# Optimization experiments

Hardware: AMD Instinct MI355X
Metric: run time of the kernel (lower is better)

Reference implementation:

```python
import jax, jax.numpy as jnp
import numpy as np

N_USER = 100000
N_ITEM = 100000
SUPP = 10000
B = 1024
L = 50
S = 256
H = 4
E = 64
HID = 64


def setup_inputs() -> dict:
    key = jax.random.key(0)
    ks = jax.random.split(key, 32)
    f32 = jnp.float32
    inp = {}
    # forward int args
    inp["x"] = jax.random.randint(ks[0], (B, 2), 0, N_USER)
    inp["src_his"] = jax.random.randint(ks[1], (B, L), 0, N_ITEM)
    inp["src_hl"] = jax.random.randint(ks[2], (B,), 0, L)
    inp["tgt_his"] = jax.random.randint(ks[3], (B, L), 0, N_ITEM)
    inp["tgt_hl"] = jax.random.randint(ks[4], (B,), 0, L)
    # precomputed neighbor sampling: [2 get_user_emb calls, H heads, B, S]
    inp["sample_idx"] = jax.random.randint(ks[5], (2, H, B, S), 0, SUPP)
    inp["supp_users"] = jax.random.randint(ks[6], (SUPP,), 0, N_USER)
    # embedding tables (xavier-ish small scale)
    inp["src_user_emb"] = jax.random.normal(ks[7], (N_USER, E), f32) * 0.1
    inp["src_item_emb"] = jax.random.normal(ks[8], (N_ITEM, E), f32) * 0.1
    inp["tgt_user_emb"] = jax.random.normal(ks[9], (N_USER, E), f32) * 0.1
    inp["tgt_item_emb"] = jax.random.normal(ks[10], (N_ITEM, E), f32) * 0.1
    # attention / aggregation weights, stored [in, out]
    s = 1.0 / np.sqrt(E)
    inp["W_att_w"] = jax.random.normal(ks[11], (E, E), f32) * s
    inp["W_att_b"] = jnp.full((E,), 0.1, f32)
    inp["W_agg_w"] = jax.random.normal(ks[12], (E, E), f32) * s
    # per-head GAT projections, batched over heads
    inp["Wq"] = jax.random.normal(ks[13], (H, E, E), f32) * s
    inp["Wk"] = jax.random.normal(ks[14], (H, E, E), f32) * s
    inp["Wv"] = jax.random.normal(ks[15], (H, E, E), f32) * s
    inp["W_out"] = jax.random.normal(ks[16], (H * E, E), f32) * (1.0 / np.sqrt(H * E))
    # scoring MLP
    inp["l1_w"] = jax.random.normal(ks[17], (2 * E, HID), f32) * (1.0 / np.sqrt(2 * E))
    inp["l1_b"] = jnp.full((HID,), 0.1, f32)
    inp["l2_w"] = jax.random.normal(ks[18], (HID, E), f32) * (1.0 / np.sqrt(HID))
    inp["l2_b"] = jnp.full((E,), 0.1, f32)
    inp["l3_w"] = jax.random.normal(ks[19], (E, 1), f32) * s
    inp["l3_b"] = jnp.full((1,), 0.1, f32)
    return inp


def reference(x, src_his, src_hl, tgt_his, tgt_hl, sample_idx, supp_users,
              src_user_emb, src_item_emb, tgt_user_emb, tgt_item_emb,
              W_att_w, W_att_b, W_agg_w, Wq, Wk, Wv, W_out,
              l1_w, l1_b, l2_w, l2_b, l3_w, l3_b):
    user_id = x[:, 0]
    item_id = x[:, 1]

    def user_fea_encode(his, hl, user_table):
        # NOTE: original always gathers from src_model.item_embedding (even for tgt)
        Lh = his.shape[1]
        valid = jnp.arange(Lh)[None, :] < hl[:, None]          # [B,L]
        hist = src_item_emb[his] * valid[..., None]             # [B,L,E], padded rows zeroed
        u = user_table[user_id]                                 # [B,E]
        keyt = jnp.tanh(hist @ W_att_w + W_att_b)               # [B,L,E]
        pad = hist.sum(-1) == 0                                 # [B,L]
        att = jnp.einsum('ble,be->bl', keyt, u)
        # faithful masked_softmax: masked scores set to 0 BEFORE exp (exp(0)=1 still contributes)
        att = jnp.where(pad, 0.0, att)
        e = jnp.exp(att)
        att = e / (jnp.sum(e, axis=1, keepdims=True) + 1e-12)
        out = jnp.einsum('bl,ble->be', att, hist)
        return out @ W_agg_w                                    # W_agg has no bias

    def get_user_emb(fea, idx):
        # idx: [H,B,S] indices into supp_users; all heads batched in one einsum chain
        neigh = tgt_user_emb[supp_users[idx]]                   # [H,B,S,E]
        q = jnp.einsum('be,heo->hbo', fea, Wq)                  # [H,B,O]
        k = jnp.einsum('hbse,heo->hbso', neigh, Wk)             # [H,B,S,O]
        attn = jax.nn.softmax(jnp.einsum('hbo,hbso->hbs', q, k), axis=-1)
        ctx = jnp.einsum('hbs,hbso->hbo', attn, k)              # weighted sum over neighbors
        g = jnp.einsum('hbo,hop->hbp', ctx, Wv)                 # [H,B,O]
        g = jnp.transpose(g, (1, 0, 2)).reshape(fea.shape[0], -1)  # concat heads -> [B,H*O]
        return g @ W_out

    user_src_fea = user_fea_encode(src_his, src_hl, src_user_emb)
    user_emb = get_user_emb(user_src_fea, sample_idx[0])
    item_emb = tgt_item_emb[item_id]
    user_tgt_fea = user_fea_encode(tgt_his, tgt_hl, tgt_user_emb)
    hybrid_tgt_emb = get_user_emb(user_tgt_fea, sample_idx[1])

    x_t = jnp.concatenate([hybrid_tgt_emb, item_emb], axis=1)
    x1_t = jnp.tanh(x_t @ l1_w + l1_b)
    x2_t = jnp.tanh(x1_t @ l2_w + l2_b)
    x3_t = (x2_t @ l3_w + l3_b).reshape(-1)

    output = jnp.sum(user_emb * item_emb, axis=1)
    out_emb_s = user_emb * item_emb
    # (output, output_t, out_emb_s, out_emb_t); train=False branch (sim/domain heads are None)
    return (output, x3_t, out_emb_s, x2_t)
```

## Files before the change

### kernel.cpp

```cpp
#include <hip/hip_runtime.h>

constexpr int B    = 1024;
constexpr int L    = 50;
constexpr int S    = 256;
constexpr int H    = 4;
constexpr int E    = 64;
constexpr int HID  = 64;
constexpr int SUPP = 10000;

__device__ __forceinline__ float lanebc(float v, int l) {
    return __int_as_float(__builtin_amdgcn_readlane(__float_as_int(v), l));
}

__global__ __launch_bounds__(256) void encode_kernel(
    const int* __restrict__ x,
    const int* __restrict__ src_his,
    const int* __restrict__ src_hl,
    const int* __restrict__ tgt_his,
    const int* __restrict__ tgt_hl,
    const float* __restrict__ item_emb,
    const float* __restrict__ src_user_emb,
    const float* __restrict__ tgt_user_emb,
    const float* __restrict__ W_att_w,
    const float* __restrict__ W_att_b,
    const float* __restrict__ W_agg_w,
    float* __restrict__ fea_out)
{
    __shared__ float sHist[L * E];
    __shared__ float sAtt[L];
    __shared__ float sPart[4][E];
    __shared__ float sOut[E];

    const int b    = blockIdx.x;
    const int call = blockIdx.y;
    const int tid  = threadIdx.x;
    const int lane = tid & 63;
    const int wave = tid >> 6;

    const int* his = call ? tgt_his : src_his;
    const int* hl  = call ? tgt_hl  : src_hl;
    const float* user_table = call ? tgt_user_emb : src_user_emb;

    float wcol[E];
#pragma unroll
    for (int i = 0; i < E; i++) wcol[i] = W_att_w[i * E + lane];

    const int uid   = x[2 * b];
    const float uv  = user_table[(size_t)uid * E + lane];
    const float bias = W_att_b[lane];
    const int hlen  = hl[b];

    for (int l = wave; l < L; l += 4) {
        const int it = his[b * L + l];
        const float hv = (l < hlen) ? item_emb[(size_t)it * E + lane] : 0.0f;
        sHist[l * E + lane] = hv;
        float a = bias;
#pragma unroll
        for (int i = 0; i < E; i++) a += lanebc(hv, i) * wcol[i];
        float part = tanhf(a) * uv;
        float hsum = hv;
#pragma unroll
        for (int off = 32; off; off >>= 1) {
            part += __shfl_xor(part, off);
            hsum += __shfl_xor(hsum, off);
        }
        if (lane == 0) sAtt[l] = (hsum == 0.0f) ? 0.0f : part;
    }
    __syncthreads();

    if (wave == 0) {
        float v = (lane < L) ? expf(sAtt[lane]) : 0.0f;
        float s = v;
#pragma unroll
        for (int off = 32; off; off >>= 1) s += __shfl_xor(s, off);
        const float denom = s + 1e-12f;
        if (lane < L) sAtt[lane] = v / denom;
    }
    __syncthreads();

    float c = 0.0f;
    for (int l = wave; l < L; l += 4) c += sAtt[l] * sHist[l * E + lane];
    sPart[wave][lane] = c;
    __syncthreads();
    if (tid < E) sOut[tid] = sPart[0][tid] + sPart[1][tid] + sPart[2][tid] + sPart[3][tid];
    __syncthreads();

    float g = 0.0f;
#pragma unroll
    for (int k = 0; k < 16; k++) {
        const int i = wave * 16 + k;
        g += sOut[i] * W_agg_w[i * E + lane];
    }
    sPart[wave][lane] = g;
    __syncthreads();
    if (wave == 0) {
        fea_out[((size_t)call * B + b) * E + lane] =
            sPart[0][lane] + sPart[1][lane] + sPart[2][lane] + sPart[3][lane];
    }
}

__global__ __launch_bounds__(256) void ksupp_kernel(
    const int* __restrict__ supp_users,
    const float* __restrict__ tgt_user_emb,
    const float* __restrict__ Wk,
    float* __restrict__ K_supp)
{
    const int tid  = threadIdx.x;
    const int lane = tid & 63;
    const int h    = tid >> 6;

    float wcol[E];
#pragma unroll
    for (int i = 0; i < E; i++) wcol[i] = Wk[h * E * E + i * E + lane];

#pragma unroll 2
    for (int j = blockIdx.x; j < SUPP; j += gridDim.x) {
        const int u = supp_users[j];
        const float ev = tgt_user_emb[(size_t)u * E + lane];
        float acc = 0.0f;
#pragma unroll
        for (int i = 0; i < E; i++) acc += lanebc(ev, i) * wcol[i];
        K_supp[((size_t)h * SUPP + j) * E + lane] = acc;
    }
}

__global__ __launch_bounds__(256) void q_kernel(
    const float* __restrict__ fea,
    const float* __restrict__ Wq,
    float* __restrict__ qout)
{
    const int tid  = threadIdx.x;
    const int lane = tid & 63;
    const int h    = tid >> 6;
    const int call = blockIdx.y;

    float wcol[E];
#pragma unroll
    for (int i = 0; i < E; i++) wcol[i] = Wq[h * E * E + i * E + lane];

    for (int b = blockIdx.x; b < B; b += gridDim.x) {
        const float fv = fea[((size_t)call * B + b) * E + lane];
        float acc = 0.0f;
#pragma unroll
        for (int i = 0; i < E; i++) acc += lanebc(fv, i) * wcol[i];
        qout[(((call * H) + h) * B + b) * E + lane] = acc;
    }
}

__global__ __launch_bounds__(256) void attn_kernel(
    const int* __restrict__ sample_idx,
    const float* __restrict__ K_supp,
    const float* __restrict__ qarr,
    const float* __restrict__ Wv,
    float* __restrict__ gout)
{
    __shared__ float sK[S * E];
    __shared__ float sP[S];
    __shared__ float sRed[8];
    __shared__ float sCtx[4][E];
    __shared__ float sC[E];
    __shared__ float sG[4][E];

    const int b    = blockIdx.x;
    const int h    = blockIdx.y;
    const int call = blockIdx.z;
    const int tid  = threadIdx.x;
    const int lane = tid & 63;
    const int wave = tid >> 6;

    const int* idx = sample_idx + (((call * H) + h) * B + b) * S;
    const float* Kh = K_supp + (size_t)h * SUPP * E;
    const float qv = qarr[(((call * H) + h) * B + b) * E + lane];

    const int s0   = wave * 64;
    const int u    = lane & 15;
    const int rsub = lane >> 4;
#pragma unroll
    for (int i = 0; i < 16; i++) {
        const int r = s0 + i * 4 + rsub;
        const int j = idx[r];
        const float4 kv = *(const float4*)(Kh + (size_t)j * E + u * 4);
        *(float4*)(sK + r * 64 + ((u ^ (r & 15)) << 2)) = kv;
    }
    __syncthreads();

    const int tmask = tid & 15;
    float acc = 0.0f;
#pragma unroll
    for (int uu = 0; uu < 16; uu++) {
        const float4 kv = *(const float4*)(sK + tid * 64 + (((uu ^ tmask)) << 2));
        acc += kv.x * lanebc(qv, 4 * uu)
             + kv.y * lanebc(qv, 4 * uu + 1)
             + kv.z * lanebc(qv, 4 * uu + 2)
             + kv.w * lanebc(qv, 4 * uu + 3);
    }

    float m = acc;
#pragma unroll
    for (int off = 32; off; off >>= 1) m = fmaxf(m, __shfl_xor(m, off));
    if (lane == 0) sRed[wave] = m;
    __syncthreads();
    const float mx = fmaxf(fmaxf(sRed[0], sRed[1]), fmaxf(sRed[2], sRed[3]));
    const float ex = expf(acc - mx);
    float sm = ex;
#pragma unroll
    for (int off = 32; off; off >>= 1) sm += __shfl_xor(sm, off);
    if (lane == 0) sRed[4 + wave] = sm;
    __syncthreads();
    const float denom = sRed[4] + sRed[5] + sRed[6] + sRed[7];
    sP[tid] = ex / denom;
    __syncthreads();

    float4 cacc = make_float4(0.0f, 0.0f, 0.0f, 0.0f);
    const int sbase = s0 + (lane >> 4) * 16;
#pragma unroll
    for (int i = 0; i < 16; i++) {
        const int s = sbase + i;
        const float ps = sP[s];
        const float4 kv = *(const float4*)(sK + s * 64 + ((u ^ (s & 15)) << 2));
        cacc.x += ps * kv.x;
        cacc.y += ps * kv.y;
        cacc.z += ps * kv.z;
        cacc.w += ps * kv.w;
    }
#pragma unroll
    for (int off = 16; off <= 32; off <<= 1) {
        cacc.x += __shfl_xor(cacc.x, off);
        cacc.y += __shfl_xor(cacc.y, off);
        cacc.z += __shfl_xor(cacc.z, off);
        cacc.w += __shfl_xor(cacc.w, off);
    }
    if (lane < 16) *(float4*)(&sCtx[wave][u * 4]) = cacc;
    __syncthreads();
    if (wave == 0) {
        sC[lane] = sCtx[0][lane] + sCtx[1][lane] + sCtx[2][lane] + sCtx[3][lane];
    }
    __syncthreads();

    const float* Wvh = Wv + h * E * E;
    float g = 0.0f;
#pragma unroll
    for (int k = 0; k < 16; k++) {
        const int c = wave * 16 + k;
        g += sC[c] * Wvh[c * E + lane];
    }
    sG[wave][lane] = g;
    __syncthreads();
    if (wave == 0) {
        gout[((size_t)(call * B) + b) * (H * E) + h * E + lane] =
            sG[0][lane] + sG[1][lane] + sG[2][lane] + sG[3][lane];
    }
}

__global__ __launch_bounds__(256) void final_kernel(
    const int* __restrict__ x,
    const float* __restrict__ tgt_item_emb,
    const float* __restrict__ gsrc,
    const float* __restrict__ gtgt,
    const float* __restrict__ W_out,
    const float* __restrict__ l1_w,
    const float* __restrict__ l1_b,
    const float* __restrict__ l2_w,
    const float* __restrict__ l2_b,
    const float* __restrict__ l3_w,
    const float* __restrict__ l3_b,
    float* __restrict__ out)
{
    __shared__ float sPart[4][E];
    __shared__ float sHyb[E];
    __shared__ float sItem[E];
    __shared__ float sX1[HID];

    const int b    = blockIdx.x;
    const int tid  = threadIdx.x;
    const int lane = tid & 63;
    const int wave = tid >> 6;

    if (tid < E) {
        const int item = x[2 * b + 1];
        sItem[tid] = tgt_item_emb[(size_t)item * E + tid];
    }

    const float* grow = (wave < 2) ? (gsrc + (size_t)b * (H * E))
                                   : (gtgt + (size_t)b * (H * E));
    const int i0 = (wave & 1) * 128;
    float acc = 0.0f;
    for (int i = i0; i < i0 + 128; i++) {
        acc += grow[i] * W_out[i * E + lane];
    }
    sPart[wave][lane] = acc;
    __syncthreads();

    if (wave == 0) {
        const float ue = sPart[0][lane] + sPart[1][lane];
        const float prod = ue * sItem[lane];
        out[2 * B + b * E + lane] = prod;
        float s = prod;
#pragma unroll
        for (int off = 32; off; off >>= 1) s += __shfl_xor(s, off);
        if (lane == 0) out[b] = s;
    }
    if (wave == 1) {
        sHyb[lane] = sPart[2][lane] + sPart[3][lane];
    }
    __syncthreads();

    if (wave == 0) {
        float a = l1_b[lane];
#pragma unroll
        for (int i = 0; i < E; i++) a += sHyb[i] * l1_w[i * HID + lane];
#pragma unroll
        for (int i = 0; i < E; i++) a += sItem[i] * l1_w[(E + i) * HID + lane];
        sX1[lane] = tanhf(a);
    }
    __syncthreads();

    if (wave == 0) {
        float a = l2_b[lane];
#pragma unroll
        for (int i = 0; i < HID; i++) a += sX1[i] * l2_w[i * E + lane];
        const float x2 = tanhf(a);
        out[2 * B + B * E + b * E + lane] = x2;
        float p = x2 * l3_w[lane];
#pragma unroll
        for (int off = 32; off; off >>= 1) p += __shfl_xor(p, off);
        if (lane == 0) out[B + b] = p + l3_b[0];
    }
}

extern "C" void kernel_launch(void* const* d_in, const int* in_sizes, int n_in,
                              void* d_out, int out_size, void* d_ws, size_t ws_size,
                              hipStream_t stream) {
    const int*   x            = (const int*)d_in[0];
    const int*   src_his      = (const int*)d_in[1];
    const int*   src_hl       = (const int*)d_in[2];
    const int*   tgt_his      = (const int*)d_in[3];
    const int*   tgt_hl       = (const int*)d_in[4];
    const int*   sample_idx   = (const int*)d_in[5];
    const int*   supp_users   = (const int*)d_in[6];
    const float* src_user_emb = (const float*)d_in[7];
    const float* src_item_emb = (const float*)d_in[8];
    const float* tgt_user_emb = (const float*)d_in[9];
    const float* tgt_item_emb = (const float*)d_in[10];
    const float* W_att_w      = (const float*)d_in[11];
    const float* W_att_b      = (const float*)d_in[12];
    const float* W_agg_w      = (const float*)d_in[13];
    const float* Wq           = (const float*)d_in[14];
    const float* Wk           = (const float*)d_in[15];
    const float* Wv           = (const float*)d_in[16];
    const float* W_out        = (const float*)d_in[17];
    const float* l1_w         = (const float*)d_in[18];
    const float* l1_b         = (const float*)d_in[19];
    const float* l2_w         = (const float*)d_in[20];
    const float* l2_b         = (const float*)d_in[21];
    const float* l3_w         = (const float*)d_in[22];
    const float* l3_b         = (const float*)d_in[23];

    float* ws      = (float*)d_ws;
    float* fea     = ws;
    float* qarr    = fea + 2 * B * E;
    float* K_supp  = qarr + 2 * H * B * E;
    float* garr    = K_supp + H * SUPP * E;
    float* out     = (float*)d_out;

    encode_kernel<<<dim3(B, 2), 256, 0, stream>>>(
        x, src_his, src_hl, tgt_his, tgt_hl, src_item_emb,
        src_user_emb, tgt_user_emb, W_att_w, W_att_b, W_agg_w, fea);
    ksupp_kernel<<<dim3(1024), 256, 0, stream>>>(
        supp_users, tgt_user_emb, Wk, K_supp);
    q_kernel<<<dim3(256, 2), 256, 0, stream>>>(
        fea, Wq, qarr);
    attn_kernel<<<dim3(B, H, 2), 256, 0, stream>>>(
        sample_idx, K_supp, qarr, Wv, garr);
    final_kernel<<<dim3(B), 256, 0, stream>>>(
        x, tgt_item_emb, garr, garr + B * H * E, W_out,
        l1_w, l1_b, l2_w, l2_b, l3_w, l3_b, out);
}
```

Measured before the change: 304.2 us.

## Fuse encode, K-support and Q projection into one kernel; keep attention keys in registers

Merges the encode, support-key projection and query projection kernels into a single launch. The support-key work runs in an extra grid row, and Q is computed directly from the encoded features held in shared memory, which removes the fea round trip through global memory and two launches. The attention kernel now keeps gathered K rows in registers and computes logits with shuffle reductions instead of staging through 64KB of shared memory. This raises occupancy but adds register pressure. The final MLP's first layer is also split across all four waves.

Result: faster. 278.6 us (-8.4%).

```diff
diff --git a/kernel.cpp b/kernel.cpp
--- a/kernel.cpp
+++ b/kernel.cpp
@@ -12,7 +12,7 @@
     return __int_as_float(__builtin_amdgcn_readlane(__float_as_int(v), l));
 }
 
-__global__ __launch_bounds__(256) void encode_kernel(
+__global__ __launch_bounds__(256) void pre_kernel(
     const int* __restrict__ x,
     const int* __restrict__ src_his,
     const int* __restrict__ src_hl,
@@ -21,11 +21,37 @@
     const float* __restrict__ item_emb,
     const float* __restrict__ src_user_emb,
     const float* __restrict__ tgt_user_emb,
+    const int* __restrict__ supp_users,
     const float* __restrict__ W_att_w,
     const float* __restrict__ W_att_b,
     const float* __restrict__ W_agg_w,
-    float* __restrict__ fea_out)
+    const float* __restrict__ Wq,
+    const float* __restrict__ Wk,
+    float* __restrict__ qout,
+    float* __restrict__ K_supp)
 {
+    const int tid  = threadIdx.x;
+    const int lane = tid & 63;
+    const int wave = tid >> 6;
+
+    if (blockIdx.y == 2) {
+        const int h = wave;
+        float wcol[E];
+#pragma unroll
+        for (int i = 0; i < E; i++) wcol[i] = Wk[h * E * E + i * E + lane];
+
+#pragma unroll 2
+        for (int j = blockIdx.x; j < SUPP; j += gridDim.x) {
+            const int u = supp_users[j];
+            const float ev = tgt_user_emb[(size_t)u * E + lane];
+            float acc = 0.0f;
+#pragma unroll
+            for (int i = 0; i < E; i++) acc += lanebc(ev, i) * wcol[i];
+            K_supp[((size_t)h * SUPP + j) * E + lane] = acc;
+        }
+        return;
+    }
+
     __shared__ float sHist[L * E];
     __shared__ float sAtt[L];
     __shared__ float sPart[4][E];
@@ -33,9 +59,6 @@
 
     const int b    = blockIdx.x;
     const int call = blockIdx.y;
-    const int tid  = threadIdx.x;
-    const int lane = tid & 63;
-    const int wave = tid >> 6;
 
     const int* his = call ? tgt_his : src_his;
     const int* hl  = call ? tgt_hl  : src_hl;
@@ -45,10 +68,10 @@
 #pragma unroll
     for (int i = 0; i < E; i++) wcol[i] = W_att_w[i * E + lane];
 
-    const int uid   = x[2 * b];
-    const float uv  = user_table[(size_t)uid * E + lane];
+    const int uid    = x[2 * b];
+    const float uv   = user_table[(size_t)uid * E + lane];
     const float bias = W_att_b[lane];
-    const int hlen  = hl[b];
+    const int hlen   = hl[b];
 
     for (int l = wave; l < L; l += 4) {
         const int it = his[b * L + l];
@@ -93,58 +116,13 @@
     }
     sPart[wave][lane] = g;
     __syncthreads();
-    if (wave == 0) {
-        fea_out[((size_t)call * B + b) * E + lane] =
-            sPart[0][lane] + sPart[1][lane] + sPart[2][lane] + sPart[3][lane];
-    }
-}
-
-__global__ __launch_bounds__(256) void ksupp_kernel(
-    const int* __restrict__ supp_users,
-    const float* __restrict__ tgt_user_emb,
-    const float* __restrict__ Wk,
-    float* __restrict__ K_supp)
-{
-    const int tid  = threadIdx.x;
-    const int lane = tid & 63;
-    const int h    = tid >> 6;
-
-    float wcol[E];
-#pragma unroll
-    for (int i = 0; i < E; i++) wcol[i] = Wk[h * E * E + i * E + lane];
-
-#pragma unroll 2
-    for (int j = blockIdx.x; j < SUPP; j += gridDim.x) {
-        const int u = supp_users[j];
-        const float ev = tgt_user_emb[(size_t)u * E + lane];
-        float acc = 0.0f;
-#pragma unroll
-        for (int i = 0; i < E; i++) acc += lanebc(ev, i) * wcol[i];
-        K_supp[((size_t)h * SUPP + j) * E + lane] = acc;
-    }
-}
-
-__global__ __launch_bounds__(256) void q_kernel(
-    const float* __restrict__ fea,
-    const float* __restrict__ Wq,
-    float* __restrict__ qout)
-{
-    const int tid  = threadIdx.x;
-    const int lane = tid & 63;
-    const int h    = tid >> 6;
-    const int call = blockIdx.y;
-
-    float wcol[E];
-#pragma unroll
-    for (int i = 0; i < E; i++) wcol[i] = Wq[h * E * E + i * E + lane];
-
-    for (int b = blockIdx.x; b < B; b += gridDim.x) {
-        const float fv = fea[((size_t)call * B + b) * E + lane];
-        float acc = 0.0f;
-#pragma unroll
-        for (int i = 0; i < E; i++) acc += lanebc(fv, i) * wcol[i];
-        qout[(((call * H) + h) * B + b) * E + lane] = acc;
-    }
+
+    const float fval = sPart[0][lane] + sPart[1][lane] + sPart[2][lane] + sPart[3][lane];
+    const float* Wqh = Wq + wave * E * E;
+    float qacc = 0.0f;
+#pragma unroll
+    for (int i = 0; i < E; i++) qacc += lanebc(fval, i) * Wqh[i * E + lane];
+    qout[(((call * H) + wave) * B + b) * E + lane] = qacc;
 }
 
 __global__ __launch_bounds__(256) void attn_kernel(
@@ -154,8 +132,6 @@
     const float* __restrict__ Wv,
     float* __restrict__ gout)
 {
-    __shared__ float sK[S * E];
-    __shared__ float sP[S];
     __shared__ float sRed[8];
     __shared__ float sCtx[4][E];
     __shared__ float sC[E];
@@ -167,61 +143,50 @@
     const int tid  = threadIdx.x;
     const int lane = tid & 63;
     const int wave = tid >> 6;
+    const int u    = lane & 15;
+    const int rsub = lane >> 4;
+    const int s0   = wave * 64;
 
     const int* idx = sample_idx + (((call * H) + h) * B + b) * S;
     const float* Kh = K_supp + (size_t)h * SUPP * E;
-    const float qv = qarr[(((call * H) + h) * B + b) * E + lane];
-
-    const int s0   = wave * 64;
-    const int u    = lane & 15;
-    const int rsub = lane >> 4;
+    const float4 qu = *(const float4*)(qarr + ((size_t)(((call * H) + h) * B + b)) * E + 4 * u);
+
+    float4 kreg[16];
+    float mylogit = 0.0f;
 #pragma unroll
     for (int i = 0; i < 16; i++) {
-        const int r = s0 + i * 4 + rsub;
-        const int j = idx[r];
-        const float4 kv = *(const float4*)(Kh + (size_t)j * E + u * 4);
-        *(float4*)(sK + r * 64 + ((u ^ (r & 15)) << 2)) = kv;
-    }
-    __syncthreads();
-
-    const int tmask = tid & 15;
-    float acc = 0.0f;
-#pragma unroll
-    for (int uu = 0; uu < 16; uu++) {
-        const float4 kv = *(const float4*)(sK + tid * 64 + (((uu ^ tmask)) << 2));
-        acc += kv.x * lanebc(qv, 4 * uu)
-             + kv.y * lanebc(qv, 4 * uu + 1)
-             + kv.z * lanebc(qv, 4 * uu + 2)
-             + kv.w * lanebc(qv, 4 * uu + 3);
-    }
-
-    float m = acc;
+        const int j = idx[s0 + 4 * i + rsub];
+        kreg[i] = *(const float4*)(Kh + (size_t)j * E + 4 * u);
+        float part = kreg[i].x * qu.x + kreg[i].y * qu.y
+                   + kreg[i].z * qu.z + kreg[i].w * qu.w;
+#pragma unroll
+        for (int off = 1; off < 16; off <<= 1) part += __shfl_xor(part, off);
+        mylogit = (u == i) ? part : mylogit;
+    }
+
+    float m = mylogit;
 #pragma unroll
     for (int off = 32; off; off >>= 1) m = fmaxf(m, __shfl_xor(m, off));
     if (lane == 0) sRed[wave] = m;
     __syncthreads();
     const float mx = fmaxf(fmaxf(sRed[0], sRed[1]), fmaxf(sRed[2], sRed[3]));
-    const float ex = expf(acc - mx);
+    const float ex = expf(mylogit - mx);
     float sm = ex;
 #pragma unroll
     for (int off = 32; off; off >>= 1) sm += __shfl_xor(sm, off);
     if (lane == 0) sRed[4 + wave] = sm;
     __syncthreads();
     const float denom = sRed[4] + sRed[5] + sRed[6] + sRed[7];
-    sP[tid] = ex / denom;
-    __syncthreads();
+    const float pval = ex / denom;
 
     float4 cacc = make_float4(0.0f, 0.0f, 0.0f, 0.0f);
-    const int sbase = s0 + (lane >> 4) * 16;
 #pragma unroll
     for (int i = 0; i < 16; i++) {
-        const int s = sbase + i;
-        const float ps = sP[s];
-        const float4 kv = *(const float4*)(sK + s * 64 + ((u ^ (s & 15)) << 2));
-        cacc.x += ps * kv.x;
-        cacc.y += ps * kv.y;
-        cacc.z += ps * kv.z;
-        cacc.w += ps * kv.w;
+        const float p = __shfl(pval, (lane & 48) + i);
+        cacc.x += p * kreg[i].x;
+        cacc.y += p * kreg[i].y;
+        cacc.z += p * kreg[i].z;
+        cacc.w += p * kreg[i].w;
     }
 #pragma unroll
     for (int off = 16; off <= 32; off <<= 1) {
@@ -305,12 +270,19 @@
     }
     __syncthreads();
 
-    if (wave == 0) {
-        float a = l1_b[lane];
-#pragma unroll
-        for (int i = 0; i < E; i++) a += sHyb[i] * l1_w[i * HID + lane];
-#pragma unroll
-        for (int i = 0; i < E; i++) a += sItem[i] * l1_w[(E + i) * HID + lane];
+    float a1 = 0.0f;
+#pragma unroll
+    for (int k = 0; k < 32; k++) {
+        const int i = wave * 32 + k;
+        const float v = (i < 64) ? sHyb[i] : sItem[i - 64];
+        a1 += v * l1_w[i * HID + lane];
+    }
+    sPart[wave][lane] = a1;
+    __syncthreads();
+
+    if (wave == 0) {
+        const float a = l1_b[lane] + sPart[0][lane] + sPart[1][lane]
+                      + sPart[2][lane] + sPart[3][lane];
         sX1[lane] = tanhf(a);
     }
     __syncthreads();
@@ -357,19 +329,15 @@
     const float* l3_b         = (const float*)d_in[23];
 
     float* ws      = (float*)d_ws;
-    float* fea     = ws;
-    float* qarr    = fea + 2 * B * E;
+    float* qarr    = ws;
     float* K_supp  = qarr + 2 * H * B * E;
     float* garr    = K_supp + H * SUPP * E;
     float* out     = (float*)d_out;
 
-    encode_kernel<<<dim3(B, 2), 256, 0, stream>>>(
+    pre_kernel<<<dim3(B, 3), 256, 0, stream>>>(
         x, src_his, src_hl, tgt_his, tgt_hl, src_item_emb,
-        src_user_emb, tgt_user_emb, W_att_w, W_att_b, W_agg_w, fea);
-    ksupp_kernel<<<dim3(1024), 256, 0, stream>>>(
-        supp_users, tgt_user_emb, Wk, K_supp);
-    q_kernel<<<dim3(256, 2), 256, 0, stream>>>(
-        fea, Wq, qarr);
+        src_user_emb, tgt_user_emb, supp_users,
+        W_att_w, W_att_b, W_agg_w, Wq, Wk, qarr, K_supp);
     attn_kernel<<<dim3(B, H, 2), 256, 0, stream>>>(
         sample_idx, K_supp, qarr, Wv, garr);
     final_kernel<<<dim3(B), 256, 0, stream>>>(
```
